# Kernel tuning notes

Measured on AMD Instinct MI355X. Metric: run time of the kernel, lower is better.

## Reference

```python
import jax, jax.numpy as jnp
import numpy as np

# dims
N, BARS, F = 1024, 64, 32          # frames, bars per frame, bar features
H, HEADS, ENC_L, FFN = 256, 8, 4, 1024
HD = H // HEADS
D, DS, DC, ML = 512, 16, 4, 8      # mamba d_model, d_state, d_conv, n_layers
DI = 2 * D                          # expand=2 -> d_inner
DR = D // 16                        # dt_rank
HID = 128                           # VIX head hidden


def _ln(x, g, b, eps=1e-5):
    m = x.mean(-1, keepdims=True)
    v = ((x - m) ** 2).mean(-1, keepdims=True)
    return (x - m) * jax.lax.rsqrt(v + eps) * g + b


def setup_inputs() -> dict:
    key = jax.random.key(0)
    ks = iter(jax.random.split(key, 64))
    r = lambda *s: jax.random.normal(next(ks), s, jnp.float32) * 0.02
    inp = {}
    inp['frames'] = jax.random.normal(next(ks), (N, BARS, F), jnp.float32)
    inp['frame_mask'] = jnp.ones((N, BARS), jnp.float32)
    # bar encoder (transformer)
    inp['in_w'] = r(F, H); inp['in_b'] = jnp.zeros((H,), jnp.float32)
    inp['pos_emb'] = r(BARS, H)
    inp['enc_qkv_w'] = r(ENC_L, H, 3 * H); inp['enc_qkv_b'] = jnp.zeros((ENC_L, 3 * H), jnp.float32)
    inp['enc_attn_out_w'] = r(ENC_L, H, H); inp['enc_attn_out_b'] = jnp.zeros((ENC_L, H), jnp.float32)
    inp['enc_ln1_g'] = jnp.ones((ENC_L, H), jnp.float32); inp['enc_ln1_b'] = jnp.zeros((ENC_L, H), jnp.float32)
    inp['enc_ffn_w1'] = r(ENC_L, H, FFN); inp['enc_ffn_b1'] = jnp.zeros((ENC_L, FFN), jnp.float32)
    inp['enc_ffn_w2'] = r(ENC_L, FFN, H); inp['enc_ffn_b2'] = jnp.zeros((ENC_L, H), jnp.float32)
    inp['enc_ln2_g'] = jnp.ones((ENC_L, H), jnp.float32); inp['enc_ln2_b'] = jnp.zeros((ENC_L, H), jnp.float32)
    # projection hidden_dim -> d_model
    inp['proj_w'] = r(H, D); inp['proj_b'] = jnp.zeros((D,), jnp.float32)
    # mamba stack (stacked over ML layers)
    inp['m_in_w'] = r(ML, D, 2 * DI)
    inp['m_conv_w'] = r(ML, DI, DC); inp['m_conv_b'] = jnp.zeros((ML, DI), jnp.float32)
    inp['m_xproj_w'] = r(ML, DI, DR + 2 * DS)
    inp['m_dt_w'] = r(ML, DR, DI)
    inp['m_dt_b'] = jnp.full((ML, DI), -4.6, jnp.float32)  # softplus(-4.6)~0.01
    inp['m_Alog'] = jnp.broadcast_to(jnp.log(jnp.arange(1, DS + 1, dtype=jnp.float32)), (ML, DI, DS)) + 0.0
    inp['m_D'] = jnp.ones((ML, DI), jnp.float32)
    inp['m_out_w'] = r(ML, DI, D)
    inp['m_ln_g'] = jnp.ones((ML, D), jnp.float32); inp['m_ln_b'] = jnp.zeros((ML, D), jnp.float32)
    # attention pooling
    inp['pool_w'] = r(D, 1); inp['pool_b'] = jnp.zeros((1,), jnp.float32)
    # VIX head
    inp['h1_w'] = r(D, HID); inp['h1_b'] = jnp.zeros((HID,), jnp.float32)
    inp['hln1_g'] = jnp.ones((HID,), jnp.float32); inp['hln1_b'] = jnp.zeros((HID,), jnp.float32)
    inp['h2_w'] = r(HID, HID); inp['h2_b'] = jnp.zeros((HID,), jnp.float32)
    inp['hln2_g'] = jnp.ones((HID,), jnp.float32); inp['hln2_b'] = jnp.zeros((HID,), jnp.float32)
    inp['h3_w'] = r(HID, 1); inp['h3_b'] = jnp.zeros((1,), jnp.float32)
    return inp


def _forward(frames, frame_mask, in_w, in_b, pos_emb, enc_qkv_w, enc_qkv_b,
             enc_attn_out_w, enc_attn_out_b, enc_ln1_g, enc_ln1_b,
             enc_ffn_w1, enc_ffn_b1, enc_ffn_w2, enc_ffn_b2, enc_ln2_g, enc_ln2_b,
             proj_w, proj_b, m_in_w, m_conv_w, m_conv_b, m_xproj_w, m_dt_w, m_dt_b,
             m_Alog, m_D, m_out_w, m_ln_g, m_ln_b, pool_w, pool_b,
             h1_w, h1_b, hln1_g, hln1_b, h2_w, h2_b, hln2_g, hln2_b, h3_w, h3_b):
    # ---- bar encoder: per-frame transformer over bars ----
    x = frames @ in_w + in_b + pos_emb                        # [N,BARS,H]
    bias = (1.0 - frame_mask)[:, None, None, :] * -1e9        # key padding mask
    scale = 1.0 / np.sqrt(HD)
    for l in range(ENC_L):
        qkv = x @ enc_qkv_w[l] + enc_qkv_b[l]
        q, k, v = jnp.split(qkv, 3, axis=-1)
        q = q.reshape(N, BARS, HEADS, HD)
        k = k.reshape(N, BARS, HEADS, HD)
        v = v.reshape(N, BARS, HEADS, HD)
        att = jnp.einsum('nqhd,nkhd->nhqk', q, k) * scale + bias
        att = jax.nn.softmax(att, axis=-1)
        o = jnp.einsum('nhqk,nkhd->nqhd', att, v).reshape(N, BARS, H)
        x = _ln(x + o @ enc_attn_out_w[l] + enc_attn_out_b[l], enc_ln1_g[l], enc_ln1_b[l])
        f = jax.nn.gelu(x @ enc_ffn_w1[l] + enc_ffn_b1[l], approximate=False) @ enc_ffn_w2[l] + enc_ffn_b2[l]
        x = _ln(x + f, enc_ln2_g[l], enc_ln2_b[l])
    m = frame_mask[..., None]
    frame_emb = (x * m).sum(1) / jnp.clip(m.sum(1), 1.0)      # [N,H] masked mean pool

    # ---- project to d_model; sequence of frames is the Mamba sequence (B=1) ----
    x = frame_emb @ proj_w + proj_b                           # [T,D], T=N
    for l in range(ML):
        res = x
        xi, z = jnp.split(x @ m_in_w[l], 2, axis=-1)          # [T,DI] each
        # causal depthwise conv1d, kernel DC
        xp = jnp.pad(xi, ((DC - 1, 0), (0, 0)))
        xw = jnp.stack([xp[k:k + N] for k in range(DC)], axis=-1)  # [T,DI,DC]
        xc = jax.nn.silu((xw * m_conv_w[l]).sum(-1) + m_conv_b[l])
        xdbl = xc @ m_xproj_w[l]                               # [T,DR+2*DS]
        dtr, Bm, Cm = xdbl[:, :DR], xdbl[:, DR:DR + DS], xdbl[:, DR + DS:]
        dt = jax.nn.softplus(dtr @ m_dt_w[l] + m_dt_b[l])      # [T,DI]
        A = -jnp.exp(m_Alog[l])                                # [DI,DS]
        dA = jnp.exp(dt[:, :, None] * A)                       # [T,DI,DS]
        dBx = dt[:, :, None] * Bm[:, None, :] * xc[:, :, None] # [T,DI,DS]

        def step(h, inp):
            dA_t, dBx_t, C_t = inp
            h = h * dA_t + dBx_t
            return h, h @ C_t                                  # y_t [DI]
        _, ys = jax.lax.scan(step, jnp.zeros((DI, DS), x.dtype), (dA, dBx, Cm))
        y = (ys + m_D[l] * xc) * jax.nn.silu(z)
        x = _ln(y @ m_out_w[l], m_ln_g[l], m_ln_b[l]) + res    # layer -> norm -> +residual

    # ---- attention pooling (no mask at this stage, matches forward()) ----
    w = jax.nn.softmax(x @ pool_w + pool_b, axis=0)            # [T,1]
    hp = (w * x).sum(0)                                        # [D]
    # ---- VIX head ----
    t = jax.nn.gelu(_ln(hp @ h1_w + h1_b, hln1_g, hln1_b), approximate=False)
    t = jax.nn.gelu(_ln(t @ h2_w + h2_b, hln2_g, hln2_b), approximate=False)
    vix = t @ h3_w + h3_b                                      # [1] (batch of 1)
    return vix, x[None]                                        # vix_pred, mamba_hidden [1,T,D]


def reference(frames, frame_mask, in_w, in_b, pos_emb, enc_qkv_w, enc_qkv_b,
              enc_attn_out_w, enc_attn_out_b, enc_ln1_g, enc_ln1_b,
              enc_ffn_w1, enc_ffn_b1, enc_ffn_w2, enc_ffn_b2, enc_ln2_g, enc_ln2_b,
              proj_w, proj_b, m_in_w, m_conv_w, m_conv_b, m_xproj_w, m_dt_w, m_dt_b,
              m_Alog, m_D, m_out_w, m_ln_g, m_ln_b, pool_w, pool_b,
              h1_w, h1_b, hln1_g, hln1_b, h2_w, h2_b, hln2_g, hln2_b, h3_w, h3_b):
    return _forward(frames, frame_mask, in_w, in_b, pos_emb, enc_qkv_w, enc_qkv_b,
                    enc_attn_out_w, enc_attn_out_b, enc_ln1_g, enc_ln1_b,
                    enc_ffn_w1, enc_ffn_b1, enc_ffn_w2, enc_ffn_b2, enc_ln2_g, enc_ln2_b,
                    proj_w, proj_b, m_in_w, m_conv_w, m_conv_b, m_xproj_w, m_dt_w, m_dt_b,
                    m_Alog, m_D, m_out_w, m_ln_g, m_ln_b, pool_w, pool_b,
                    h1_w, h1_b, hln1_g, hln1_b, h2_w, h2_b, hln2_g, hln2_b, h3_w, h3_b)
```

## Files before the change

kernel.cpp:

```cpp
#include <hip/hip_runtime.h>
#include <math.h>

#define ACT_NONE 0
#define ACT_GELU 1
#define ACT_SOFTPLUS 2

template<int ACT>
__device__ __forceinline__ float act_apply(float x){
  if (ACT == ACT_GELU)     return 0.5f * x * (1.0f + erff(x * 0.70710678118654752f));
  if (ACT == ACT_SOFTPLUS) return fmaxf(x, 0.0f) + log1pf(expf(-fabsf(x)));
  return x;
}

__device__ __forceinline__ unsigned short f2bf(float x){
  unsigned u = __float_as_uint(x);
  u = u + 0x7FFFu + ((u >> 16) & 1u);
  return (unsigned short)(u >> 16);
}
__device__ __forceinline__ float bf2f(unsigned short b){
  return __uint_as_float(((unsigned)b) << 16);
}
__device__ __forceinline__ void bfsplit(float x, unsigned short &hi, unsigned short &lo){
  hi = f2bf(x);
  lo = f2bf(x - bf2f(hi));
}

typedef __attribute__((ext_vector_type(8))) short v8s;
typedef __attribute__((ext_vector_type(4))) float v4f;

template<int ACT, int OUT>
__global__ __launch_bounds__(256) void gemm_bf16x2_kernel(
    const unsigned short* __restrict__ Ahi, const unsigned short* __restrict__ Alo,
    const unsigned short* __restrict__ Bhi, const unsigned short* __restrict__ Blo,
    const float* __restrict__ bias, float* __restrict__ C,
    unsigned short* __restrict__ Chi, unsigned short* __restrict__ Clo,
    int K, int lda, int ldb, int ldc)
{
  __shared__ unsigned short As[2][128][40];
  __shared__ unsigned short Bs[2][128][40];
  const int tid = threadIdx.x;
  const int m0 = blockIdx.y * 128;
  const int n0 = blockIdx.x * 128;
  const int w = tid >> 6, lane = tid & 63;
  const int wm = (w & 1) * 64, wn = (w >> 1) * 64;
  const int fm = lane & 15, fq = lane >> 4;
  const int r = tid >> 1, h = tid & 1;

  const unsigned short* pAh = Ahi + (size_t)(m0 + r) * lda + h * 16;
  const unsigned short* pAl = Alo + (size_t)(m0 + r) * lda + h * 16;
  const unsigned short* pBh = Bhi + (size_t)(n0 + r) * ldb + h * 16;
  const unsigned short* pBl = Blo + (size_t)(n0 + r) * ldb + h * 16;

  v4f acc[4][4];
#pragma unroll
  for (int i = 0; i < 4; i++)
#pragma unroll
    for (int j = 0; j < 4; j++) acc[i][j] = (v4f){0.f, 0.f, 0.f, 0.f};

  uint4 ah0 = *(const uint4*)(pAh),     ah1 = *(const uint4*)(pAh + 8);
  uint4 al0 = *(const uint4*)(pAl),     al1 = *(const uint4*)(pAl + 8);
  uint4 bh0 = *(const uint4*)(pBh),     bh1 = *(const uint4*)(pBh + 8);
  uint4 bl0 = *(const uint4*)(pBl),     bl1 = *(const uint4*)(pBl + 8);

  for (int k0 = 0; k0 < K; k0 += 32) {
    __syncthreads();
    *(uint4*)&As[0][r][h * 16]     = ah0;
    *(uint4*)&As[0][r][h * 16 + 8] = ah1;
    *(uint4*)&As[1][r][h * 16]     = al0;
    *(uint4*)&As[1][r][h * 16 + 8] = al1;
    *(uint4*)&Bs[0][r][h * 16]     = bh0;
    *(uint4*)&Bs[0][r][h * 16 + 8] = bh1;
    *(uint4*)&Bs[1][r][h * 16]     = bl0;
    *(uint4*)&Bs[1][r][h * 16 + 8] = bl1;
    __syncthreads();

    if (k0 + 32 < K) {
      int kn = k0 + 32;
      ah0 = *(const uint4*)(pAh + kn); ah1 = *(const uint4*)(pAh + kn + 8);
      al0 = *(const uint4*)(pAl + kn); al1 = *(const uint4*)(pAl + kn + 8);
      bh0 = *(const uint4*)(pBh + kn); bh1 = *(const uint4*)(pBh + kn + 8);
      bl0 = *(const uint4*)(pBl + kn); bl1 = *(const uint4*)(pBl + kn + 8);
    }

    v8s ah[4], al[4];
#pragma unroll
    for (int i = 0; i < 4; i++) {
      ah[i] = *(const v8s*)&As[0][wm + i * 16 + fm][fq * 8];
      al[i] = *(const v8s*)&As[1][wm + i * 16 + fm][fq * 8];
    }
#pragma unroll
    for (int j = 0; j < 4; j++) {
      v8s bh = *(const v8s*)&Bs[0][wn + j * 16 + fm][fq * 8];
      v8s bl = *(const v8s*)&Bs[1][wn + j * 16 + fm][fq * 8];
#pragma unroll
      for (int i = 0; i < 4; i++) {
        acc[i][j] = __builtin_amdgcn_mfma_f32_16x16x32_bf16(ah[i], bh, acc[i][j], 0, 0, 0);
        acc[i][j] = __builtin_amdgcn_mfma_f32_16x16x32_bf16(ah[i], bl, acc[i][j], 0, 0, 0);
        acc[i][j] = __builtin_amdgcn_mfma_f32_16x16x32_bf16(al[i], bh, acc[i][j], 0, 0, 0);
      }
    }
  }

#pragma unroll
  for (int i = 0; i < 4; i++)
#pragma unroll
    for (int j = 0; j < 4; j++) {
      int col = n0 + wn + j * 16 + fm;
      float bv = bias ? bias[col] : 0.0f;
#pragma unroll
      for (int reg = 0; reg < 4; reg++) {
        int row = m0 + wm + i * 16 + fq * 4 + reg;
        float v = acc[i][j][reg] + bv;
        v = act_apply<ACT>(v);
        size_t idx = (size_t)row * ldc + col;
        if (OUT == 0) C[idx] = v;
        else { unsigned short hi, lo; bfsplit(v, hi, lo); Chi[idx] = hi; Clo[idx] = lo; }
      }
    }
}

__global__ __launch_bounds__(512) void gemm_ln_kernel(
    const unsigned short* __restrict__ Ahi, const unsigned short* __restrict__ Alo,
    const unsigned short* __restrict__ Bhi, const unsigned short* __restrict__ Blo,
    const float* __restrict__ bias,
    const float* __restrict__ g, const float* __restrict__ beta,
    unsigned short* __restrict__ Xhi, unsigned short* __restrict__ Xlo,
    int K, int lda, int ldb)
{
  __shared__ unsigned short As[2][64][40];
  __shared__ unsigned short Bs[2][256][40];
  __shared__ float rs[64][9];
  __shared__ float ms[64][2];
  const int tid = threadIdx.x;
  const int m0 = blockIdx.x * 64;
  const int w = tid >> 6, lane = tid & 63;
  const int fm = lane & 15, fq = lane >> 4;
  const int a_pl  = tid >> 8;
  const int a_row = (tid >> 2) & 63;
  const int a_c   = tid & 3;
  const int b_row = tid >> 2;
  const int b_c   = tid & 3;

  v4f acc[4][2];
#pragma unroll
  for (int i = 0; i < 4; i++)
#pragma unroll
    for (int j = 0; j < 2; j++) acc[i][j] = (v4f){0.f, 0.f, 0.f, 0.f};

  for (int k0 = 0; k0 < K; k0 += 32) {
    __syncthreads();
    {
      const unsigned short* asrc = (a_pl ? Alo : Ahi) + (size_t)(m0 + a_row) * lda + k0 + a_c * 8;
      *(uint4*)&As[a_pl][a_row][a_c * 8] = *(const uint4*)asrc;
    }
    *(uint4*)&Bs[0][b_row      ][b_c * 8] = *(const uint4*)(Bhi + (size_t)(b_row      ) * ldb + k0 + b_c * 8);
    *(uint4*)&Bs[0][b_row + 128][b_c * 8] = *(const uint4*)(Bhi + (size_t)(b_row + 128) * ldb + k0 + b_c * 8);
    *(uint4*)&Bs[1][b_row      ][b_c * 8] = *(const uint4*)(Blo + (size_t)(b_row      ) * ldb + k0 + b_c * 8);
    *(uint4*)&Bs[1][b_row + 128][b_c * 8] = *(const uint4*)(Blo + (size_t)(b_row + 128) * ldb + k0 + b_c * 8);
    __syncthreads();

    v8s ah[4], al[4];
#pragma unroll
    for (int i = 0; i < 4; i++) {
      ah[i] = *(const v8s*)&As[0][i * 16 + fm][fq * 8];
      al[i] = *(const v8s*)&As[1][i * 16 + fm][fq * 8];
    }
#pragma unroll
    for (int j = 0; j < 2; j++) {
      v8s bhf = *(const v8s*)&Bs[0][w * 32 + j * 16 + fm][fq * 8];
      v8s blf = *(const v8s*)&Bs[1][w * 32 + j * 16 + fm][fq * 8];
#pragma unroll
      for (int i = 0; i < 4; i++) {
        acc[i][j] = __builtin_amdgcn_mfma_f32_16x16x32_bf16(ah[i], bhf, acc[i][j], 0, 0, 0);
        acc[i][j] = __builtin_amdgcn_mfma_f32_16x16x32_bf16(ah[i], blf, acc[i][j], 0, 0, 0);
        acc[i][j] = __builtin_amdgcn_mfma_f32_16x16x32_bf16(al[i], bhf, acc[i][j], 0, 0, 0);
      }
    }
  }

#pragma unroll
  for (int i = 0; i < 4; i++)
#pragma unroll
    for (int j = 0; j < 2; j++) {
      int cl = w * 32 + j * 16 + fm;
      float bv = bias[cl];
#pragma unroll
      for (int reg = 0; reg < 4; reg++) {
        int rl = i * 16 + fq * 4 + reg;
        size_t idx = (size_t)(m0 + rl) * 256 + cl;
        acc[i][j][reg] += bv + bf2f(Xhi[idx]) + bf2f(Xlo[idx]);
      }
    }
#pragma unroll
  for (int i = 0; i < 4; i++)
#pragma unroll
    for (int reg = 0; reg < 4; reg++) {
      float s = acc[i][0][reg] + acc[i][1][reg];
      s += __shfl_xor(s, 1); s += __shfl_xor(s, 2);
      s += __shfl_xor(s, 4); s += __shfl_xor(s, 8);
      if (fm == 0) rs[i * 16 + fq * 4 + reg][w] = s;
    }
  __syncthreads();
  if (tid < 64) {
    float s = 0.0f;
#pragma unroll
    for (int q = 0; q < 8; q++) s += rs[tid][q];
    ms[tid][0] = s * (1.0f / 256.0f);
  }
  __syncthreads();
#pragma unroll
  for (int i = 0; i < 4; i++)
#pragma unroll
    for (int reg = 0; reg < 4; reg++) {
      int rl = i * 16 + fq * 4 + reg;
      float mean = ms[rl][0];
      float d0 = acc[i][0][reg] - mean;
      float d1 = acc[i][1][reg] - mean;
      float s = d0 * d0 + d1 * d1;
      s += __shfl_xor(s, 1); s += __shfl_xor(s, 2);
      s += __shfl_xor(s, 4); s += __shfl_xor(s, 8);
      if (fm == 0) rs[rl][w] = s;
    }
  __syncthreads();
  if (tid < 64) {
    float s = 0.0f;
#pragma unroll
    for (int q = 0; q < 8; q++) s += rs[tid][q];
    ms[tid][1] = rsqrtf(s * (1.0f / 256.0f) + 1e-5f);
  }
  __syncthreads();
#pragma unroll
  for (int i = 0; i < 4; i++)
#pragma unroll
    for (int j = 0; j < 2; j++) {
      int cl = w * 32 + j * 16 + fm;
      float gv = g[cl], bv = beta[cl];
#pragma unroll
      for (int reg = 0; reg < 4; reg++) {
        int rl = i * 16 + fq * 4 + reg;
        float t = (acc[i][j][reg] - ms[rl][0]) * ms[rl][1] * gv + bv;
        size_t idx = (size_t)(m0 + rl) * 256 + cl;
        unsigned short hi, lo; bfsplit(t, hi, lo);
        Xhi[idx] = hi; Xlo[idx] = lo;
      }
    }
}

__global__ __launch_bounds__(256) void wsplit_kernel(
    const float* __restrict__ W, unsigned short* __restrict__ Whi,
    unsigned short* __restrict__ Wlo, int K, int N, size_t wstride, size_t ostride)
{
  __shared__ float tile[32][33];
  const float* Wl = W + blockIdx.z * wstride;
  unsigned short* Whl = Whi + blockIdx.z * ostride;
  unsigned short* Wll = Wlo + blockIdx.z * ostride;
  int k0 = blockIdx.y * 32, n0 = blockIdx.x * 32;
  int t = threadIdx.x;
  int tn = t & 31, tk8 = t >> 5;
#pragma unroll
  for (int i = 0; i < 4; i++) {
    int k = tk8 + i * 8;
    tile[k][tn] = Wl[(size_t)(k0 + k) * N + n0 + tn];
  }
  __syncthreads();
  int tk = t & 31, tn8 = t >> 5;
#pragma unroll
  for (int i = 0; i < 4; i++) {
    int n = tn8 + i * 8;
    float v = tile[tk][n];
    unsigned short hi, lo; bfsplit(v, hi, lo);
    size_t idx = (size_t)(n0 + n) * K + k0 + tk;
    Whl[idx] = hi; Wll[idx] = lo;
  }
}

template<int ACT, int POS, int SPLIT>
__global__ __launch_bounds__(256) void gemm128_kernel(
    const float* __restrict__ A, const float* __restrict__ W,
    const float* __restrict__ bias, const float* __restrict__ pos,
    float* __restrict__ C, unsigned short* __restrict__ Chi, unsigned short* __restrict__ Clo,
    int K, int lda, int ldw, int ldc)
{
  __shared__ float As[16][128];
  __shared__ float Ws[16][128];
  const int tid = threadIdx.x;
  const int m0 = blockIdx.y * 128;
  const int n0 = blockIdx.x * 128;
  const int tx = tid & 15, ty = tid >> 4;
  const int ar = tid >> 2, ak = (tid & 3) * 4;
  const int wk = tid >> 5, wn = (tid & 31) * 4;

  float acc[8][8];
#pragma unroll
  for (int i = 0; i < 8; i++)
#pragma unroll
    for (int j = 0; j < 8; j++) acc[i][j] = 0.0f;

  for (int k0 = 0; k0 < K; k0 += 16) {
    float4 a0 = *(const float4*)(A + (size_t)(m0 + ar)      * lda + k0 + ak);
    float4 a1 = *(const float4*)(A + (size_t)(m0 + ar + 64) * lda + k0 + ak);
    float4 w0 = *(const float4*)(W + (size_t)(k0 + wk)     * ldw + n0 + wn);
    float4 w1 = *(const float4*)(W + (size_t)(k0 + wk + 8) * ldw + n0 + wn);
    __syncthreads();
    As[ak + 0][ar] = a0.x; As[ak + 1][ar] = a0.y; As[ak + 2][ar] = a0.z; As[ak + 3][ar] = a0.w;
    As[ak + 0][ar + 64] = a1.x; As[ak + 1][ar + 64] = a1.y; As[ak + 2][ar + 64] = a1.z; As[ak + 3][ar + 64] = a1.w;
    *(float4*)&Ws[wk][wn] = w0;
    *(float4*)&Ws[wk + 8][wn] = w1;
    __syncthreads();
#pragma unroll
    for (int k = 0; k < 16; k++) {
      float4 xa = *(float4*)&As[k][ty * 8];
      float4 xb = *(float4*)&As[k][ty * 8 + 4];
      float4 y0 = *(float4*)&Ws[k][tx * 8];
      float4 y1 = *(float4*)&Ws[k][tx * 8 + 4];
      float a8[8] = {xa.x, xa.y, xa.z, xa.w, xb.x, xb.y, xb.z, xb.w};
      float b8[8] = {y0.x, y0.y, y0.z, y0.w, y1.x, y1.y, y1.z, y1.w};
#pragma unroll
      for (int i = 0; i < 8; i++)
#pragma unroll
        for (int j = 0; j < 8; j++) acc[i][j] = fmaf(a8[i], b8[j], acc[i][j]);
    }
  }
#pragma unroll
  for (int i = 0; i < 8; i++) {
    int row = m0 + ty * 8 + i;
    float* cp = C + (size_t)row * ldc + n0 + tx * 8;
    float v[8];
#pragma unroll
    for (int j = 0; j < 8; j++) {
      float t = acc[i][j];
      int col = n0 + tx * 8 + j;
      if (bias) t += bias[col];
      if (POS)  t += pos[(row & 63) * 256 + col];
      t = act_apply<ACT>(t);
      v[j] = t;
      if (SPLIT) {
        unsigned short hi, lo; bfsplit(t, hi, lo);
        size_t idx = (size_t)row * ldc + col;
        Chi[idx] = hi; Clo[idx] = lo;
      }
    }
    *(float4*)cp       = make_float4(v[0], v[1], v[2], v[3]);
    *(float4*)(cp + 4) = make_float4(v[4], v[5], v[6], v[7]);
  }
}

template<int ACT>
__global__ __launch_bounds__(256) void gemm64_kernel(
    const float* __restrict__ A, const float* __restrict__ W,
    const float* __restrict__ bias, float* __restrict__ C,
    int K, int lda, int ldw, int ldc)
{
  __shared__ float As[16][64];
  __shared__ float Ws[16][64];
  const int tid = threadIdx.x;
  const int m0 = blockIdx.y * 64;
  const int n0 = blockIdx.x * 64;
  const int tx = tid & 15, ty = tid >> 4;
  const int ar = tid >> 2, ak = (tid & 3) * 4;
  const int wk = tid >> 4, wn = (tid & 15) * 4;

  float acc[4][4];
#pragma unroll
  for (int i = 0; i < 4; i++)
#pragma unroll
    for (int j = 0; j < 4; j++) acc[i][j] = 0.0f;

  float4 a0 = *(const float4*)(A + (size_t)(m0 + ar) * lda + ak);
  float4 w0 = *(const float4*)(W + (size_t)wk * ldw + n0 + wn);

  for (int k0 = 0; k0 < K; k0 += 16) {
    __syncthreads();
    As[ak + 0][ar] = a0.x; As[ak + 1][ar] = a0.y; As[ak + 2][ar] = a0.z; As[ak + 3][ar] = a0.w;
    *(float4*)&Ws[wk][wn] = w0;
    __syncthreads();
    if (k0 + 16 < K) {
      a0 = *(const float4*)(A + (size_t)(m0 + ar) * lda + k0 + 16 + ak);
      w0 = *(const float4*)(W + (size_t)(k0 + 16 + wk) * ldw + n0 + wn);
    }
#pragma unroll
    for (int k = 0; k < 16; k++) {
      float4 xa = *(float4*)&As[k][ty * 4];
      float4 yb = *(float4*)&Ws[k][tx * 4];
      float a4[4] = {xa.x, xa.y, xa.z, xa.w};
      float b4[4] = {yb.x, yb.y, yb.z, yb.w};
#pragma unroll
      for (int i = 0; i < 4; i++)
#pragma unroll
        for (int j = 0; j < 4; j++) acc[i][j] = fmaf(a4[i], b4[j], acc[i][j]);
    }
  }
#pragma unroll
  for (int i = 0; i < 4; i++) {
    float* cp = C + (size_t)(m0 + ty * 4 + i) * ldc + n0 + tx * 4;
    float v[4];
#pragma unroll
    for (int j = 0; j < 4; j++) {
      float t = acc[i][j];
      if (bias) t += bias[n0 + tx * 4 + j];
      v[j] = act_apply<ACT>(t);
    }
    *(float4*)cp = make_float4(v[0], v[1], v[2], v[3]);
  }
}

__global__ __launch_bounds__(64) void attn_fused_kernel(
    const float* __restrict__ QKVc, const float* __restrict__ mask,
    unsigned short* __restrict__ AThi, unsigned short* __restrict__ ATlo, int n0)
{
  int bid = blockIdx.x;
  int nl = bid >> 3;
  int h = bid & 7;
  int n = n0 + nl;
  int tid = threadIdx.x;
  int tx = tid & 7, ty = tid >> 3;
  __shared__ float QKP[4352];
  float (*Qt)[68] = (float(*)[68])QKP;
  float (*Kt)[68] = (float(*)[68])(QKP + 32 * 68);
  float (*Pt)[68] = (float(*)[68])QKP;
  __shared__ float Vs[64][36];
  __shared__ float bs[64];
  const float* base = QKVc + (size_t)nl * (64 * 768);
#pragma unroll
  for (int i = 0; i < 32; i++) {
    int idx = tid + i * 64;
    int bar = idx >> 5, c = idx & 31;
    Qt[c][bar] = base[bar * 768 + h * 32 + c];
    Kt[c][bar] = base[bar * 768 + 256 + h * 32 + c];
    Vs[bar][c] = base[bar * 768 + 512 + h * 32 + c];
  }
  bs[tid] = (1.0f - mask[n * 64 + tid]) * -1e9f;
  __syncthreads();
  float acc[8][8] = {};
  for (int c = 0; c < 32; c++) {
    float4 ax = *(float4*)&Qt[c][ty * 8];
    float4 ay = *(float4*)&Qt[c][ty * 8 + 4];
    float4 bx = *(float4*)&Kt[c][tx * 8];
    float4 by = *(float4*)&Kt[c][tx * 8 + 4];
    float a8[8] = {ax.x, ax.y, ax.z, ax.w, ay.x, ay.y, ay.z, ay.w};
    float b8[8] = {bx.x, bx.y, bx.z, bx.w, by.x, by.y, by.z, by.w};
#pragma unroll
    for (int i = 0; i < 8; i++)
#pragma unroll
      for (int j = 0; j < 8; j++) acc[i][j] = fmaf(a8[i], b8[j], acc[i][j]);
  }
  __syncthreads();
  const float scale = 0.17677669529663687f;
#pragma unroll
  for (int i = 0; i < 8; i++) {
    float s[8];
    float mx = -3.0e38f;
#pragma unroll
    for (int j = 0; j < 8; j++) { s[j] = acc[i][j] * scale + bs[tx * 8 + j]; mx = fmaxf(mx, s[j]); }
#pragma unroll
    for (int off = 1; off < 8; off <<= 1) mx = fmaxf(mx, __shfl_xor(mx, off));
    float sum = 0.0f;
#pragma unroll
    for (int j = 0; j < 8; j++) { s[j] = expf(s[j] - mx); sum += s[j]; }
#pragma unroll
    for (int off = 1; off < 8; off <<= 1) sum += __shfl_xor(sum, off);
    float inv = 1.0f / sum;
#pragma unroll
    for (int j = 0; j < 8; j++) Pt[tx * 8 + j][ty * 8 + i] = s[j] * inv;
  }
  __syncthreads();
  float o[8][4] = {};
  for (int j = 0; j < 64; j++) {
    float4 px = *(float4*)&Pt[j][ty * 8];
    float4 py = *(float4*)&Pt[j][ty * 8 + 4];
    float4 v  = *(float4*)&Vs[j][tx * 4];
    float p8[8] = {px.x, px.y, px.z, px.w, py.x, py.y, py.z, py.w};
#pragma unroll
    for (int i = 0; i < 8; i++) {
      o[i][0] = fmaf(p8[i], v.x, o[i][0]);
      o[i][1] = fmaf(p8[i], v.y, o[i][1]);
      o[i][2] = fmaf(p8[i], v.z, o[i][2]);
      o[i][3] = fmaf(p8[i], v.w, o[i][3]);
    }
  }
#pragma unroll
  for (int i = 0; i < 8; i++) {
    size_t base_o = (size_t)(nl * 64 + ty * 8 + i) * 256 + h * 32 + tx * 4;
#pragma unroll
    for (int c = 0; c < 4; c++) {
      unsigned short hi, lo; bfsplit(o[i][c], hi, lo);
      AThi[base_o + c] = hi; ATlo[base_o + c] = lo;
    }
  }
}

__global__ __launch_bounds__(256) void ln_res_kernel(
    const float* __restrict__ a, const float* __restrict__ b,
    const float* __restrict__ g, const float* __restrict__ beta,
    float* __restrict__ o, int Wd)
{
  int wave = threadIdx.x >> 6;
  int lane = threadIdx.x & 63;
  int row = blockIdx.x * 4 + wave;
  int P = Wd >> 6;
  const float* ar = a + (size_t)row * Wd;
  const float* br = b + (size_t)row * Wd;
  float v[8];
  float s = 0.0f;
  for (int i = 0; i < P; i++) { float x = ar[lane + i * 64]; v[i] = x; s += x; }
#pragma unroll
  for (int off = 32; off; off >>= 1) s += __shfl_xor(s, off);
  float mean = s / Wd;
  float vs = 0.0f;
  for (int i = 0; i < P; i++) { float d = v[i] - mean; vs += d * d; }
#pragma unroll
  for (int off = 32; off; off >>= 1) vs += __shfl_xor(vs, off);
  float rstd = rsqrtf(vs / Wd + 1e-5f);
  for (int i = 0; i < P; i++) {
    int col = lane + i * 64;
    o[(size_t)row * Wd + col] = (v[i] - mean) * rstd * g[col] + beta[col] + br[col];
  }
}

__global__ __launch_bounds__(256) void mean_kernel(
    const unsigned short* __restrict__ Xhi, const unsigned short* __restrict__ Xlo,
    const float* __restrict__ mask, float* __restrict__ FE, int n0)
{
  int n = blockIdx.x;
  int c = threadIdx.x;
  float s = 0.0f, ms = 0.0f;
  for (int bar = 0; bar < 64; bar++) {
    float mk = mask[(n0 + n) * 64 + bar];
    size_t idx = (size_t)(n * 64 + bar) * 256 + c;
    s = fmaf(bf2f(Xhi[idx]) + bf2f(Xlo[idx]), mk, s);
    ms += mk;
  }
  FE[(n0 + n) * 256 + c] = s / fmaxf(ms, 1.0f);
}

__global__ __launch_bounds__(256) void conv_kernel(
    const float* __restrict__ XZ, const float* __restrict__ w,
    const float* __restrict__ b, float* __restrict__ XC)
{
  int idx = blockIdx.x * 256 + threadIdx.x;
  int t = idx >> 10, c = idx & 1023;
  float acc = b[c];
  const float* wc = w + c * 4;
#pragma unroll
  for (int k = 0; k < 4; k++) {
    int tt = t + k - 3;
    if (tt >= 0) acc = fmaf(XZ[(size_t)tt * 2048 + c], wc[k], acc);
  }
  XC[idx] = acc / (1.0f + expf(-acc));
}

#define NCH 32
#define CLEN 32

__global__ __launch_bounds__(256) void scan1_kernel(
    const float* __restrict__ DT, const float* __restrict__ XC,
    const float* __restrict__ XDBL, const float* __restrict__ Alog,
    float* __restrict__ HEND, float* __restrict__ PPR)
{
  int j = blockIdx.x >> 2;
  int c = (blockIdx.x & 3) * 256 + threadIdx.x;
  int t0 = j * CLEN;
  __shared__ float Bs[CLEN][16];
  for (int i = threadIdx.x; i < CLEN * 16; i += 256) {
    int r = i >> 4, s = i & 15;
    Bs[r][s] = XDBL[(t0 + r) * 64 + 32 + s];
  }
  float A[16], h[16], Pp[16];
#pragma unroll
  for (int s = 0; s < 16; s++) {
    A[s] = -expf(Alog[c * 16 + s]);
    h[s] = 0.0f; Pp[s] = 1.0f;
  }
  __syncthreads();
  for (int tt = 0; tt < CLEN; tt++) {
    int t = t0 + tt;
    float dtv = DT[(size_t)t * 1024 + c];
    float u = dtv * XC[(size_t)t * 1024 + c];
#pragma unroll
    for (int s = 0; s < 16; s++) {
      float e = expf(dtv * A[s]);
      h[s] = fmaf(h[s], e, u * Bs[tt][s]);
      Pp[s] *= e;
    }
  }
#pragma unroll
  for (int s = 0; s < 16; s++) {
    HEND[(size_t)(j * 1024 + c) * 16 + s] = h[s];
    PPR [(size_t)(j * 1024 + c) * 16 + s] = Pp[s];
  }
}

__global__ __launch_bounds__(256) void scan2_kernel(
    const float* __restrict__ HEND, const float* __restrict__ PPR, float* __restrict__ CIN)
{
  int id = blockIdx.x * 256 + threadIdx.x;
  float carry = 0.0f;
  for (int j = 0; j < NCH; j++) {
    CIN[j * 16384 + id] = carry;
    carry = fmaf(PPR[j * 16384 + id], carry, HEND[j * 16384 + id]);
  }
}

__global__ __launch_bounds__(256) void scan3_kernel(
    const float* __restrict__ DT, const float* __restrict__ XC,
    const float* __restrict__ XDBL, const float* __restrict__ Alog,
    const float* __restrict__ CIN, const float* __restrict__ mD,
    const float* __restrict__ XZ, float* __restrict__ Y)
{
  int j = blockIdx.x >> 2;
  int c = (blockIdx.x & 3) * 256 + threadIdx.x;
  int t0 = j * CLEN;
  __shared__ float Bs[CLEN][16], Cs[CLEN][16];
  for (int i = threadIdx.x; i < CLEN * 16; i += 256) {
    int r = i >> 4, s = i & 15;
    Bs[r][s] = XDBL[(t0 + r) * 64 + 32 + s];
    Cs[r][s] = XDBL[(t0 + r) * 64 + 48 + s];
  }
  float A[16], h[16];
#pragma unroll
  for (int s = 0; s < 16; s++) {
    A[s] = -expf(Alog[c * 16 + s]);
    h[s] = CIN[(size_t)(j * 1024 + c) * 16 + s];
  }
  float dval = mD[c];
  __syncthreads();
  for (int tt = 0; tt < CLEN; tt++) {
    int t = t0 + tt;
    float dtv = DT[(size_t)t * 1024 + c];
    float xcv = XC[(size_t)t * 1024 + c];
    float u = dtv * xcv;
    float y = 0.0f;
#pragma unroll
    for (int s = 0; s < 16; s++) {
      float e = expf(dtv * A[s]);
      h[s] = fmaf(h[s], e, u * Bs[tt][s]);
      y = fmaf(h[s], Cs[tt][s], y);
    }
    float z = XZ[(size_t)t * 2048 + 1024 + c];
    float sz = z / (1.0f + expf(-z));
    Y[(size_t)t * 1024 + c] = (y + dval * xcv) * sz;
  }
}

__global__ __launch_bounds__(1024) void pool1_kernel(
    const float* __restrict__ XM, const float* __restrict__ pw,
    const float* __restrict__ pb, float* __restrict__ PW)
{
  int t = threadIdx.x;
  float s = pb[0];
  for (int i = 0; i < 512; i++) s = fmaf(XM[(size_t)t * 512 + i], pw[i], s);
  __shared__ float red[1024];
  red[t] = s;
  __syncthreads();
  for (int off = 512; off > 0; off >>= 1) {
    if (t < off) red[t] = fmaxf(red[t], red[t + off]);
    __syncthreads();
  }
  float mx = red[0];
  __syncthreads();
  float e = expf(s - mx);
  red[t] = e;
  __syncthreads();
  for (int off = 512; off > 0; off >>= 1) {
    if (t < off) red[t] = red[t] + red[t + off];
    __syncthreads();
  }
  PW[t] = e / red[0];
}

__global__ __launch_bounds__(256) void pool2_kernel(
    const float* __restrict__ XM, const float* __restrict__ PW, float* __restrict__ HP)
{
  int hcol = blockIdx.x * 256 + threadIdx.x;
  float s = 0.0f;
  for (int tn = 0; tn < 1024; tn++) s = fmaf(PW[tn], XM[(size_t)tn * 512 + hcol], s);
  HP[hcol] = s;
}

__device__ __forceinline__ float blk_reduce_sum_128(float v, float* red){
  int t = threadIdx.x;
#pragma unroll
  for (int off = 32; off; off >>= 1) v += __shfl_xor(v, off);
  __syncthreads();
  if ((t & 63) == 0) red[t >> 6] = v;
  __syncthreads();
  return red[0] + red[1];
}

__global__ __launch_bounds__(128) void head_kernel(
    const float* __restrict__ HP, const float* __restrict__ h1w, const float* __restrict__ h1b,
    const float* __restrict__ g1, const float* __restrict__ be1,
    const float* __restrict__ h2w, const float* __restrict__ h2b,
    const float* __restrict__ g2, const float* __restrict__ be2,
    const float* __restrict__ h3w, const float* __restrict__ h3b,
    float* __restrict__ out)
{
  __shared__ float t1[128];
  __shared__ float red[2];
  int i = threadIdx.x;
  float s = h1b[i];
  for (int k = 0; k < 512; k++) s = fmaf(HP[k], h1w[k * 128 + i], s);
  float mean = blk_reduce_sum_128(s, red) * (1.0f / 128.0f);
  float d = s - mean;
  float var = blk_reduce_sum_128(d * d, red) * (1.0f / 128.0f);
  float x1 = d * rsqrtf(var + 1e-5f) * g1[i] + be1[i];
  x1 = 0.5f * x1 * (1.0f + erff(x1 * 0.70710678118654752f));
  t1[i] = x1;
  __syncthreads();
  s = h2b[i];
  for (int k = 0; k < 128; k++) s = fmaf(t1[k], h2w[k * 128 + i], s);
  mean = blk_reduce_sum_128(s, red) * (1.0f / 128.0f);
  d = s - mean;
  var = blk_reduce_sum_128(d * d, red) * (1.0f / 128.0f);
  float x2 = d * rsqrtf(var + 1e-5f) * g2[i] + be2[i];
  x2 = 0.5f * x2 * (1.0f + erff(x2 * 0.70710678118654752f));
  float tot = blk_reduce_sum_128(x2 * h3w[i], red);
  if (i == 0) out[0] = tot + h3b[0];
}

__global__ __launch_bounds__(256) void copyx_kernel(const float* __restrict__ XM, float* __restrict__ out){
  int i = blockIdx.x * 256 + threadIdx.x;
  out[1 + i] = XM[i];
}

extern "C" void kernel_launch(void* const* d_in, const int* in_sizes, int n_in,
                              void* d_out, int out_size, void* d_ws, size_t ws_size,
                              hipStream_t stream)
{
  const float* frames   = (const float*)d_in[0];
  const float* fmask    = (const float*)d_in[1];
  const float* in_w     = (const float*)d_in[2];
  const float* in_b     = (const float*)d_in[3];
  const float* pos_emb  = (const float*)d_in[4];
  const float* qkv_w    = (const float*)d_in[5];
  const float* qkv_b    = (const float*)d_in[6];
  const float* ao_w     = (const float*)d_in[7];
  const float* ao_b     = (const float*)d_in[8];
  const float* ln1_g    = (const float*)d_in[9];
  const float* ln1_b    = (const float*)d_in[10];
  const float* ffn_w1   = (const float*)d_in[11];
  const float* ffn_b1   = (const float*)d_in[12];
  const float* ffn_w2   = (const float*)d_in[13];
  const float* ffn_b2   = (const float*)d_in[14];
  const float* ln2_g    = (const float*)d_in[15];
  const float* ln2_b    = (const float*)d_in[16];
  const float* proj_w   = (const float*)d_in[17];
  const float* proj_b   = (const float*)d_in[18];
  const float* m_in_w   = (const float*)d_in[19];
  const float* m_conv_w = (const float*)d_in[20];
  const float* m_conv_b = (const float*)d_in[21];
  const float* m_xproj_w= (const float*)d_in[22];
  const float* m_dt_w   = (const float*)d_in[23];
  const float* m_dt_b   = (const float*)d_in[24];
  const float* m_Alog   = (const float*)d_in[25];
  const float* m_D      = (const float*)d_in[26];
  const float* m_out_w  = (const float*)d_in[27];
  const float* m_ln_g   = (const float*)d_in[28];
  const float* m_ln_b   = (const float*)d_in[29];
  const float* pool_w   = (const float*)d_in[30];
  const float* pool_b   = (const float*)d_in[31];
  const float* h1_w     = (const float*)d_in[32];
  const float* h1_b     = (const float*)d_in[33];
  const float* hg1      = (const float*)d_in[34];
  const float* hb1      = (const float*)d_in[35];
  const float* h2_w     = (const float*)d_in[36];
  const float* h2_b     = (const float*)d_in[37];
  const float* hg2      = (const float*)d_in[38];
  const float* hb2      = (const float*)d_in[39];
  const float* h3_w     = (const float*)d_in[40];
  const float* h3_b     = (const float*)d_in[41];
  float* out = (float*)d_out;

  float* ws = (float*)d_ws;
  float* B  = ws;
  float* QF = B;
  unsigned short* AThi = (unsigned short*)(B + 12582912);
  unsigned short* ATlo = AThi + 4194304;
  unsigned short* MIDhi = (unsigned short*)B;
  unsigned short* MIDlo = MIDhi + 16777216;

  unsigned short* Xhi = (unsigned short*)(ws + 16777216);
  unsigned short* Xlo = Xhi + 4194304;

  unsigned short* Wqkv_hi = (unsigned short*)(ws + 20971520);
  unsigned short* Wqkv_lo = Wqkv_hi + 786432;
  unsigned short* Wao_hi  = Wqkv_lo + 786432;
  unsigned short* Wao_lo  = Wao_hi + 262144;
  unsigned short* Wf1_hi  = Wao_lo + 262144;
  unsigned short* Wf1_lo  = Wf1_hi + 1048576;
  unsigned short* Wf2_hi  = Wf1_lo + 1048576;
  unsigned short* Wf2_lo  = Wf2_hi + 1048576;

  float* FE = ws + 24117248;
  float* XM = FE + 262144;
  float* PW = XM + 524288;
  float* HP = PW + 2048;

  float* XZ   = B;
  float* XC   = B + 2097152;
  float* DT   = B + 3145728;
  float* XDBL = B + 4194304;
  float* Y    = B + 4259840;
  float* TMP  = B + 5308416;
  float* HEND = B + 5832704;
  float* PPR  = B + 6356992;
  float* CIN  = B + 6881280;

  wsplit_kernel<<<dim3(24,8,4),256,0,stream>>>(qkv_w, Wqkv_hi, Wqkv_lo, 256, 768, 196608, 196608);
  wsplit_kernel<<<dim3(8,8,4),256,0,stream>>>(ao_w, Wao_hi, Wao_lo, 256, 256, 65536, 65536);
  wsplit_kernel<<<dim3(32,8,4),256,0,stream>>>(ffn_w1, Wf1_hi, Wf1_lo, 256, 1024, 262144, 262144);
  wsplit_kernel<<<dim3(8,32,4),256,0,stream>>>(ffn_w2, Wf2_hi, Wf2_lo, 1024, 256, 262144, 262144);

  for (int ch = 0; ch < 4; ch++) {
    int n0 = ch * 256;
    const float* fch = frames + (size_t)n0 * 64 * 32;
    gemm128_kernel<ACT_NONE,1,1><<<dim3(2,128),256,0,stream>>>(
        fch, in_w, in_b, pos_emb, QF, Xhi, Xlo, 32, 32, 256, 256);
    for (int l = 0; l < 4; l++) {
      gemm_bf16x2_kernel<ACT_NONE,0><<<dim3(6,128),256,0,stream>>>(
          Xhi, Xlo, Wqkv_hi + l*196608, Wqkv_lo + l*196608, qkv_b + l*768,
          QF, nullptr, nullptr, 256, 256, 256, 768);
      attn_fused_kernel<<<2048,64,0,stream>>>(QF, fmask, AThi, ATlo, n0);
      gemm_ln_kernel<<<256,512,0,stream>>>(
          AThi, ATlo, Wao_hi + l*65536, Wao_lo + l*65536, ao_b + l*256,
          ln1_g + l*256, ln1_b + l*256, Xhi, Xlo, 256, 256, 256);
      gemm_bf16x2_kernel<ACT_GELU,2><<<dim3(8,128),256,0,stream>>>(
          Xhi, Xlo, Wf1_hi + l*262144, Wf1_lo + l*262144, ffn_b1 + l*1024,
          nullptr, MIDhi, MIDlo, 256, 256, 256, 1024);
      gemm_ln_kernel<<<256,512,0,stream>>>(
          MIDhi, MIDlo, Wf2_hi + l*262144, Wf2_lo + l*262144, ffn_b2 + l*256,
          ln2_g + l*256, ln2_b + l*256, Xhi, Xlo, 1024, 1024, 1024);
    }
    mean_kernel<<<256,256,0,stream>>>(Xhi, Xlo, fmask, FE, n0);
  }

  gemm64_kernel<ACT_NONE><<<dim3(8,16),256,0,stream>>>(FE, proj_w, proj_b, XM, 256, 256, 512, 512);

  for (int l = 0; l < 8; l++) {
    gemm64_kernel<ACT_NONE><<<dim3(32,16),256,0,stream>>>(
        XM, m_in_w + (size_t)l*512*2048, nullptr, XZ, 512, 512, 2048, 2048);
    conv_kernel<<<4096,256,0,stream>>>(XZ, m_conv_w + l*1024*4, m_conv_b + l*1024, XC);
    gemm64_kernel<ACT_NONE><<<dim3(1,16),256,0,stream>>>(
        XC, m_xproj_w + (size_t)l*1024*64, nullptr, XDBL, 1024, 1024, 64, 64);
    gemm64_kernel<ACT_SOFTPLUS><<<dim3(16,16),256,0,stream>>>(
        XDBL, m_dt_w + (size_t)l*32*1024, m_dt_b + l*1024, DT, 32, 64, 1024, 1024);
    scan1_kernel<<<128,256,0,stream>>>(DT, XC, XDBL, m_Alog + l*16384, HEND, PPR);
    scan2_kernel<<<64,256,0,stream>>>(HEND, PPR, CIN);
    scan3_kernel<<<128,256,0,stream>>>(DT, XC, XDBL, m_Alog + l*16384, CIN, m_D + l*1024, XZ, Y);
    gemm64_kernel<ACT_NONE><<<dim3(8,16),256,0,stream>>>(
        Y, m_out_w + (size_t)l*1024*512, nullptr, TMP, 1024, 1024, 512, 512);
    ln_res_kernel<<<256,256,0,stream>>>(TMP, XM, m_ln_g + l*512, m_ln_b + l*512, XM, 512);
  }

  pool1_kernel<<<1,1024,0,stream>>>(XM, pool_w, pool_b, PW);
  pool2_kernel<<<2,256,0,stream>>>(XM, PW, HP);
  head_kernel<<<1,128,0,stream>>>(HP, h1_w, h1_b, hg1, hb1, h2_w, h2_b, hg2, hb2, h3_w, h3_b, out);
  copyx_kernel<<<2048,256,0,stream>>>(XM, out);
}
```

Measured before the change: 5.392 ms.

## Run Mamba in-projection on bf16x2 MFMA GEMM and swap encoder grid axes

The Mamba input projection (1024x512 by 512x2048) moves from the fp32 FMA gemm64 kernel to the split-bf16 MFMA GEMM. The projection and LayerNorm-residual kernels now also emit hi/lo bf16 copies of XM, and the in_proj weights are split each layer. The bf16 GEMM's grid axes are swapped so consecutive blocks walk along M, which may improve weight reuse in cache. The cost is extra split-output stores and a per-layer weight-split kernel, with precision close to fp32 via hi/lo splitting.

```diff
diff --git a/kernel.cpp b/kernel.cpp
--- a/kernel.cpp
+++ b/kernel.cpp
@@ -39,8 +39,8 @@
   __shared__ unsigned short As[2][128][40];
   __shared__ unsigned short Bs[2][128][40];
   const int tid = threadIdx.x;
-  const int m0 = blockIdx.y * 128;
-  const int n0 = blockIdx.x * 128;
+  const int m0 = blockIdx.x * 128;
+  const int n0 = blockIdx.y * 128;
   const int w = tid >> 6, lane = tid & 63;
   const int wm = (w & 1) * 64, wn = (w >> 1) * 64;
   const int fm = lane & 15, fq = lane >> 4;
@@ -345,10 +345,11 @@
   }
 }
 
-template<int ACT>
+template<int ACT, int SPLIT>
 __global__ __launch_bounds__(256) void gemm64_kernel(
     const float* __restrict__ A, const float* __restrict__ W,
     const float* __restrict__ bias, float* __restrict__ C,
+    unsigned short* __restrict__ Chi, unsigned short* __restrict__ Clo,
     int K, int lda, int ldw, int ldc)
 {
   __shared__ float As[16][64];
@@ -392,13 +393,20 @@
   }
 #pragma unroll
   for (int i = 0; i < 4; i++) {
-    float* cp = C + (size_t)(m0 + ty * 4 + i) * ldc + n0 + tx * 4;
+    int row = m0 + ty * 4 + i;
+    float* cp = C + (size_t)row * ldc + n0 + tx * 4;
     float v[4];
 #pragma unroll
     for (int j = 0; j < 4; j++) {
       float t = acc[i][j];
       if (bias) t += bias[n0 + tx * 4 + j];
-      v[j] = act_apply<ACT>(t);
+      t = act_apply<ACT>(t);
+      v[j] = t;
+      if (SPLIT) {
+        unsigned short hi, lo; bfsplit(t, hi, lo);
+        size_t idx = (size_t)row * ldc + n0 + tx * 4 + j;
+        Chi[idx] = hi; Clo[idx] = lo;
+      }
     }
     *(float4*)cp = make_float4(v[0], v[1], v[2], v[3]);
   }
@@ -492,7 +500,8 @@
 __global__ __launch_bounds__(256) void ln_res_kernel(
     const float* __restrict__ a, const float* __restrict__ b,
     const float* __restrict__ g, const float* __restrict__ beta,
-    float* __restrict__ o, int Wd)
+    float* __restrict__ o, unsigned short* __restrict__ ohi, unsigned short* __restrict__ olo,
+    int Wd)
 {
   int wave = threadIdx.x >> 6;
   int lane = threadIdx.x & 63;
@@ -513,7 +522,11 @@
   float rstd = rsqrtf(vs / Wd + 1e-5f);
   for (int i = 0; i < P; i++) {
     int col = lane + i * 64;
-    o[(size_t)row * Wd + col] = (v[i] - mean) * rstd * g[col] + beta[col] + br[col];
+    float t = (v[i] - mean) * rstd * g[col] + beta[col] + br[col];
+    size_t idx = (size_t)row * Wd + col;
+    o[idx] = t;
+    unsigned short hi, lo; bfsplit(t, hi, lo);
+    ohi[idx] = hi; olo[idx] = lo;
   }
 }
 
@@ -795,6 +808,8 @@
   float* XM = FE + 262144;
   float* PW = XM + 524288;
   float* HP = PW + 2048;
+  unsigned short* XMhi = (unsigned short*)(ws + 24906752);
+  unsigned short* XMlo = XMhi + 524288;
 
   float* XZ   = B;
   float* XC   = B + 2097152;
@@ -805,6 +820,8 @@
   float* HEND = B + 5832704;
   float* PPR  = B + 6356992;
   float* CIN  = B + 6881280;
+  unsigned short* WINhi = (unsigned short*)(B + 7500000);
+  unsigned short* WINlo = WINhi + 1048576;
 
   wsplit_kernel<<<dim3(24,8,4),256,0,stream>>>(qkv_w, Wqkv_hi, Wqkv_lo, 256, 768, 196608, 196608);
   wsplit_kernel<<<dim3(8,8,4),256,0,stream>>>(ao_w, Wao_hi, Wao_lo, 256, 256, 65536, 65536);
@@ -817,14 +834,14 @@
     gemm128_kernel<ACT_NONE,1,1><<<dim3(2,128),256,0,stream>>>(
         fch, in_w, in_b, pos_emb, QF, Xhi, Xlo, 32, 32, 256, 256);
     for (int l = 0; l < 4; l++) {
-      gemm_bf16x2_kernel<ACT_NONE,0><<<dim3(6,128),256,0,stream>>>(
+      gemm_bf16x2_kernel<ACT_NONE,0><<<dim3(128,6),256,0,stream>>>(
           Xhi, Xlo, Wqkv_hi + l*196608, Wqkv_lo + l*196608, qkv_b + l*768,
           QF, nullptr, nullptr, 256, 256, 256, 768);
       attn_fused_kernel<<<2048,64,0,stream>>>(QF, fmask, AThi, ATlo, n0);
       gemm_ln_kernel<<<256,512,0,stream>>>(
           AThi, ATlo, Wao_hi + l*65536, Wao_lo + l*65536, ao_b + l*256,
           ln1_g + l*256, ln1_b + l*256, Xhi, Xlo, 256, 256, 256);
-      gemm_bf16x2_kernel<ACT_GELU,2><<<dim3(8,128),256,0,stream>>>(
+      gemm_bf16x2_kernel<ACT_GELU,2><<<dim3(128,8),256,0,stream>>>(
           Xhi, Xlo, Wf1_hi + l*262144, Wf1_lo + l*262144, ffn_b1 + l*1024,
           nullptr, MIDhi, MIDlo, 256, 256, 256, 1024);
       gemm_ln_kernel<<<256,512,0,stream>>>(
@@ -834,22 +851,25 @@
     mean_kernel<<<256,256,0,stream>>>(Xhi, Xlo, fmask, FE, n0);
   }
 
-  gemm64_kernel<ACT_NONE><<<dim3(8,16),256,0,stream>>>(FE, proj_w, proj_b, XM, 256, 256, 512, 512);
+  gemm64_kernel<ACT_NONE,1><<<dim3(8,16),256,0,stream>>>(
+      FE, proj_w, proj_b, XM, XMhi, XMlo, 256, 256, 512, 512);
 
   for (int l = 0; l < 8; l++) {
-    gemm64_kernel<ACT_NONE><<<dim3(32,16),256,0,stream>>>(
-        XM, m_in_w + (size_t)l*512*2048, nullptr, XZ, 512, 512, 2048, 2048);
+    wsplit_kernel<<<dim3(64,16,1),256,0,stream>>>(
+        m_in_w + (size_t)l*512*2048, WINhi, WINlo, 512, 2048, 0, 0);
+    gemm_bf16x2_kernel<ACT_NONE,0><<<dim3(8,16),256,0,stream>>>(
+        XMhi, XMlo, WINhi, WINlo, nullptr, XZ, nullptr, nullptr, 512, 512, 512, 2048);
     conv_kernel<<<4096,256,0,stream>>>(XZ, m_conv_w + l*1024*4, m_conv_b + l*1024, XC);
-    gemm64_kernel<ACT_NONE><<<dim3(1,16),256,0,stream>>>(
-        XC, m_xproj_w + (size_t)l*1024*64, nullptr, XDBL, 1024, 1024, 64, 64);
-    gemm64_kernel<ACT_SOFTPLUS><<<dim3(16,16),256,0,stream>>>(
-        XDBL, m_dt_w + (size_t)l*32*1024, m_dt_b + l*1024, DT, 32, 64, 1024, 1024);
+    gemm64_kernel<ACT_NONE,0><<<dim3(1,16),256,0,stream>>>(
+        XC, m_xproj_w + (size_t)l*1024*64, nullptr, XDBL, nullptr, nullptr, 1024, 1024, 64, 64);
+    gemm64_kernel<ACT_SOFTPLUS,0><<<dim3(16,16),256,0,stream>>>(
+        XDBL, m_dt_w + (size_t)l*32*1024, m_dt_b + l*1024, DT, nullptr, nullptr, 32, 64, 1024, 1024);
     scan1_kernel<<<128,256,0,stream>>>(DT, XC, XDBL, m_Alog + l*16384, HEND, PPR);
     scan2_kernel<<<64,256,0,stream>>>(HEND, PPR, CIN);
     scan3_kernel<<<128,256,0,stream>>>(DT, XC, XDBL, m_Alog + l*16384, CIN, m_D + l*1024, XZ, Y);
-    gemm64_kernel<ACT_NONE><<<dim3(8,16),256,0,stream>>>(
-        Y, m_out_w + (size_t)l*1024*512, nullptr, TMP, 1024, 1024, 512, 512);
-    ln_res_kernel<<<256,256,0,stream>>>(TMP, XM, m_ln_g + l*512, m_ln_b + l*512, XM, 512);
+    gemm64_kernel<ACT_NONE,0><<<dim3(8,16),256,0,stream>>>(
+        Y, m_out_w + (size_t)l*1024*512, nullptr, TMP, nullptr, nullptr, 1024, 1024, 512, 512);
+    ln_res_kernel<<<256,256,0,stream>>>(TMP, XM, m_ln_g + l*512, m_ln_b + l*512, XM, XMhi, XMlo, 512);
   }
 
   pool1_kernel<<<1,1024,0,stream>>>(XM, pool_w, pool_b, PW);
```

Measured after the change: 5.314 ms. No clear change (-1.4%).
